# Kernel optimization log

Hardware: AMD Instinct MI355X
Metric: run time of the kernel (lower is better)

## Reference

```python
import jax, jax.numpy as jnp
import numpy as np

# MSEObserver config: bit=4, symmetric=False, ch_axis=-1
QMIN, QMAX = 0, 15          # asymmetric int4: [0, 2^4 - 1]
NUM = 100                   # range-grid resolution
EPS = np.float32(np.finfo(np.float32).eps)


def setup_inputs() -> dict:
    key = jax.random.key(0)
    x_orig = jax.random.normal(key, (1024, 4096), dtype=jnp.float32)
    return {"x_orig": x_orig}


def _search_2d(x):
    # per-tensor (ch_axis == -1) 2D grid search over (range, zero_point)
    x_min = jnp.min(x)
    x_max = jnp.max(x)
    xrange = x_max - x_min
    qrange = float(QMAX - QMIN)
    zps = jnp.arange(QMIN, QMAX + 1, dtype=jnp.float32)  # [Z] candidate zp shifts

    def step(carry, i):
        best_score, best_min, best_max = carry
        tmp_max = xrange / NUM * i           # tmp_min == 0
        tmp_delta = tmp_max / qrange
        new_min = jnp.maximum(-zps * tmp_delta, x_min)           # [Z]
        new_max = jnp.minimum(tmp_max - zps * tmp_delta, x_max)  # [Z]
        # calculate_qparams (asymmetric)
        min_neg = jnp.minimum(new_min, 0.0)
        max_pos = jnp.maximum(new_max, 0.0)
        scale = jnp.maximum((max_pos - min_neg) / qrange, EPS)   # [Z]
        zp = jnp.clip(QMIN - jnp.round(min_neg / scale), QMIN, QMAX)  # [Z]
        s = scale[:, None, None]
        z = zp[:, None, None]
        # fake_quantize_per_tensor_affine, vectorized over Z candidates
        xq = (jnp.clip(jnp.round(x[None] / s) + z, QMIN, QMAX) - z) * s  # [Z,T,D]
        score = jnp.mean(jnp.square(xq - x[None]), axis=(1, 2))  # [Z], lp_loss p=2
        j = jnp.argmin(score)
        sc = score[j]
        better = sc < best_score
        best_min = jnp.where(better, new_min[j], best_min)
        best_max = jnp.where(better, new_max[j], best_max)
        best_score = jnp.minimum(best_score, sc)
        return (best_score, best_min, best_max), None

    init = (jnp.float32(1e10), x_min, x_max)
    iis = jnp.arange(1, NUM + 1, dtype=jnp.float32)
    (best_score, best_min, best_max), _ = jax.lax.scan(step, init, iis)
    return best_min, best_max


def reference(x_orig) -> jnp.ndarray:
    # randn input => one_side_dist == 'no', symmetric == False -> perform_2D_search
    x = x_orig.astype(jnp.float32)
    best_min, best_max = _search_2d(x)
    # buffer update: min_val = min(+inf, best_min), max_val = max(-inf, best_max)
    return jnp.stack([best_min, best_max])
```

## Files before the change

kernel.cpp:

```cpp
#include <hip/hip_runtime.h>
#include <math.h>

#define NUM_I 100
#define NZ    16
#define NCAND (NUM_I * NZ)
#define NBL   8192
#define G2    256
#define BLK   1024
#define SLICE 16384
#define BPT   (NBL / BLK)
#define F32_EPS 1.1920928955078125e-07f
#define AGENT __HIP_MEMORY_SCOPE_AGENT

struct WSL {
    unsigned* ctrs;
    double*   score;
    float*    pmin; float* pmax;
    float4*   params; float2* ranges; float* mm;
    double*   scoreFB;
    size_t    small_needed;
};

__host__ __device__ static inline WSL make_ws(char* w0) {
    WSL L; char* w = w0;
    L.ctrs   = (unsigned*)w; w += 64;
    L.score  = (double*)w;   w += sizeof(double) * NCAND;
    L.pmin   = (float*)w;    w += sizeof(float) * G2;
    L.pmax   = (float*)w;    w += sizeof(float) * G2;
    L.params = (float4*)w;   w += sizeof(float4) * NCAND;
    L.ranges = (float2*)w;   w += sizeof(float2) * NCAND;
    L.mm     = (float*)w;    w += sizeof(float) * 4;
    size_t head = (size_t)(w - w0);
    L.small_needed = (head + 15) & ~(size_t)15;
    L.scoreFB = L.score;
    return L;
}

static __device__ __forceinline__ float rfl_f(float v) {
    return __int_as_float(__builtin_amdgcn_readfirstlane(__float_as_int(v)));
}
static __device__ __forceinline__ double agent_load_f64(const double* p) {
    return __hip_atomic_load(p, __ATOMIC_RELAXED, AGENT);
}
static __device__ __forceinline__ int bin_loc(float v, float lo, float invw) {
    int b = (int)floorf((v - lo) * invw);
    return min(max(b, 0), NBL - 1);
}
static __device__ __forceinline__ void gbar(unsigned* ctr, int nblk) {
    __syncthreads();
    if (threadIdx.x == 0) {
        __hip_atomic_fetch_add(ctr, 1u, __ATOMIC_ACQ_REL, AGENT);
        while (__hip_atomic_load(ctr, __ATOMIC_RELAXED, AGENT) < (unsigned)nblk)
            __builtin_amdgcn_s_sleep(8);
        (void)__hip_atomic_load(ctr, __ATOMIC_ACQUIRE, AGENT);
    }
    __syncthreads();
}

__global__ __launch_bounds__(BLK, 4) void k_fused(const float* __restrict__ x, int n4,
                                                  char* wsbase, float* __restrict__ out) {
    WSL L = make_ws(wsbase);
    __shared__ __align__(16) float ssort[SLICE];
    __shared__ __align__(8) unsigned short Cs[NBL + 2];
    __shared__ __align__(16) double S1p[NBL];
    __shared__ double   dpart[BLK];
    __shared__ unsigned upart[BLK];
    __shared__ double   stot[1];
    __shared__ float    sxm[2];
    __shared__ int      islast;
    unsigned* Htmp = (unsigned*)S1p;
    const int tid = threadIdx.x, blk = blockIdx.x;
    const float4* x4 = (const float4*)x;
    const int per4 = (n4 + G2 - 1) / G2;
    const int beg4 = blk * per4, end4 = min(beg4 + per4, n4);
    const int len = (end4 > beg4) ? (end4 - beg4) * 4 : 0;

    {
        int gtid = blk * BLK + tid;
        if (gtid < NCAND) L.score[gtid] = 0.0;
        float* rmin = (float*)dpart; float* rmax = rmin + BLK;
        float lmin = 3.0e38f, lmax = -3.0e38f;
        for (int i = beg4 + tid; i < end4; i += BLK) {
            float4 v = x4[i];
            lmin = fminf(lmin, fminf(fminf(v.x, v.y), fminf(v.z, v.w)));
            lmax = fmaxf(lmax, fmaxf(fmaxf(v.x, v.y), fmaxf(v.z, v.w)));
        }
        rmin[tid] = lmin; rmax[tid] = lmax;
        __syncthreads();
        for (int s = BLK / 2; s > 0; s >>= 1) {
            if (tid < s) {
                rmin[tid] = fminf(rmin[tid], rmin[tid + s]);
                rmax[tid] = fmaxf(rmax[tid], rmax[tid + s]);
            }
            __syncthreads();
        }
        if (tid == 0) { L.pmin[blk] = rmin[0]; L.pmax[blk] = rmax[0]; }
    }
    gbar(&L.ctrs[0], G2);

    {
        float* rmin = (float*)dpart; float* rmax = rmin + BLK;
        float lmin = (tid < G2) ? L.pmin[tid] : 3.0e38f;
        float lmax = (tid < G2) ? L.pmax[tid] : -3.0e38f;
        rmin[tid] = lmin; rmax[tid] = lmax;
        __syncthreads();
        for (int s = BLK / 2; s > 0; s >>= 1) {
            if (tid < s) {
                rmin[tid] = fminf(rmin[tid], rmin[tid + s]);
                rmax[tid] = fmaxf(rmax[tid], rmax[tid + s]);
            }
            __syncthreads();
        }
        if (tid == 0) { sxm[0] = rmin[0]; sxm[1] = rmax[0]; }
        __syncthreads();
    }
    const float x_min = sxm[0], x_max = sxm[1];
    const float rangef = x_max - x_min;
    const float lo = x_min;
    const float invw = (rangef > 0.0f) ? ((float)NBL / rangef) : 0.0f;

    if (len > 0) {
        for (int b = tid; b < NBL; b += BLK) Htmp[b] = 0u;
        __syncthreads();
        for (int i = beg4 + tid; i < end4; i += BLK) {
            float4 v = x4[i];
            atomicAdd(&Htmp[bin_loc(v.x, lo, invw)], 1u);
            atomicAdd(&Htmp[bin_loc(v.y, lo, invw)], 1u);
            atomicAdd(&Htmp[bin_loc(v.z, lo, invw)], 1u);
            atomicAdd(&Htmp[bin_loc(v.w, lo, invw)], 1u);
        }
        __syncthreads();
        unsigned cl[BPT]; unsigned ps = 0;
        #pragma unroll
        for (int k = 0; k < BPT; k++) { cl[k] = Htmp[tid * BPT + k]; ps += cl[k]; }
        upart[tid] = ps;
        __syncthreads();
        for (int off = 1; off < BLK; off <<= 1) {
            unsigned v = (tid >= off) ? upart[tid - off] : 0u;
            __syncthreads();
            upart[tid] += v;
            __syncthreads();
        }
        unsigned run = upart[tid] - ps;
        #pragma unroll
        for (int k = 0; k < BPT; k++) {
            int b = tid * BPT + k;
            Cs[b] = (unsigned short)run;
            Htmp[b] = run;
            run += cl[k];
        }
        if (tid == BLK - 1) Cs[NBL] = (unsigned short)run;
        __syncthreads();
        for (int i = beg4 + tid; i < end4; i += BLK) {
            float4 v = x4[i];
            unsigned p;
            p = atomicAdd(&Htmp[bin_loc(v.x, lo, invw)], 1u); ssort[p] = v.x;
            p = atomicAdd(&Htmp[bin_loc(v.y, lo, invw)], 1u); ssort[p] = v.y;
            p = atomicAdd(&Htmp[bin_loc(v.z, lo, invw)], 1u); ssort[p] = v.z;
            p = atomicAdd(&Htmp[bin_loc(v.w, lo, invw)], 1u); ssort[p] = v.w;
        }
        __syncthreads();
        for (int k = 0; k < BPT; k++) {
            int b = tid + k * BLK;
            unsigned st = Cs[b], en = Cs[b + 1];
            double s1 = 0.0;
            for (unsigned i = st; i < en; i++) s1 += (double)ssort[i];
            S1p[b] = s1;
        }
        __syncthreads();
        double l1[BPT];
        double a1 = 0.0;
        #pragma unroll
        for (int k = 0; k < BPT; k++) { l1[k] = S1p[tid * BPT + k]; a1 += l1[k]; }
        dpart[tid] = a1;
        __syncthreads();
        for (int off = 1; off < BLK; off <<= 1) {
            double v1 = (tid >= off) ? dpart[tid - off] : 0.0;
            __syncthreads();
            dpart[tid] += v1;
            __syncthreads();
        }
        double b1 = dpart[tid] - a1;
        #pragma unroll
        for (int k = 0; k < BPT; k++) {
            int b = tid * BPT + k;
            S1p[b] = b1; b1 += l1[k];
        }
        if (tid == BLK - 1) stot[0] = dpart[BLK - 1];
        __syncthreads();

        const double totS1 = stot[0];
        for (int q = 0; q < (NCAND + BLK - 1) / BLK; q++) {
            int cand = q * BLK + ((tid + blk) & (BLK - 1));
            if (cand >= NCAND) continue;
            int zi; double sd;
            {
#pragma clang fp contract(off)
                float step = rangef / 100.0f;
                int ii = cand >> 4, z = cand & 15;
                float fi = (float)(ii + 1);
                float tmp_max   = step * fi;
                float tmp_delta = tmp_max / 15.0f;
                float t = (float)z * tmp_delta;
                float new_min = fmaxf(-t, x_min);
                float new_max = fminf(tmp_max - t, x_max);
                float min_neg = fminf(new_min, 0.0f);
                float max_pos = fmaxf(new_max, 0.0f);
                float scale = fmaxf((max_pos - min_neg) / 15.0f, F32_EPS);
                float zp = 0.0f - rintf(min_neg / scale);
                zp = fminf(fmaxf(zp, 0.0f), 15.0f);
                zi = (int)zp; sd = (double)scale;
            }
            double prevC = 0.0, prev1 = 0.0, sc = 0.0;
            for (int j = 0; j <= 15; j++) {
                double Cc, C1;
                if (j < 15) {
                    double td = ((double)(j - zi) + 0.5) * sd;
                    float tf = (float)td;
                    int bf = bin_loc(tf, lo, invw);
                    unsigned st = Cs[bf], en = Cs[bf + 1];
                    unsigned cnt = 0; double s1 = 0.0;
                    unsigned i = st;
                    for (; i < en && (i & 3u); i++) {
                        float v = ssort[i];
                        if (v < tf) { cnt++; s1 += (double)v; }
                    }
                    for (; i + 4u <= en; i += 4u) {
                        float4 v4 = *reinterpret_cast<const float4*>(&ssort[i]);
                        float m0 = (v4.x < tf) ? v4.x : 0.0f;
                        float m1 = (v4.y < tf) ? v4.y : 0.0f;
                        float m2 = (v4.z < tf) ? v4.z : 0.0f;
                        float m3 = (v4.w < tf) ? v4.w : 0.0f;
                        cnt += (v4.x < tf); cnt += (v4.y < tf);
                        cnt += (v4.z < tf); cnt += (v4.w < tf);
                        s1 += (double)((m0 + m1) + (m2 + m3));
                    }
                    for (; i < en; i++) {
                        float v = ssort[i];
                        if (v < tf) { cnt++; s1 += (double)v; }
                    }
                    Cc = (double)st + (double)cnt;
                    C1 = S1p[bf] + s1;
                } else {
                    Cc = (double)len; C1 = totS1;
                }
                double ms = (double)(j - zi) * sd;
                sc += ms * (ms * (Cc - prevC) - 2.0 * (C1 - prev1));
                prevC = Cc; prev1 = C1;
            }
            atomicAdd(&L.score[cand], sc);
        }
    }

    __syncthreads();
    if (tid == 0) {
        __threadfence();
        unsigned old = atomicAdd(&L.ctrs[1], 1u);
        islast = (old == gridDim.x - 1) ? 1 : 0;
    }
    __syncthreads();
    if (!islast) return;
    __threadfence();

    double* bsc = dpart;
    int*    bix = (int*)upart;
    double best = 1.0e300; int bidx = 0x7fffffff;
    for (int c = tid; c < NCAND; c += BLK) {
        double sc = agent_load_f64(&L.score[c]);
        if (sc < best) { best = sc; bidx = c; }
    }
    bsc[tid] = best; bix[tid] = bidx;
    __syncthreads();
    for (int s = BLK / 2; s > 0; s >>= 1) {
        if (tid < s) {
            double so = bsc[tid + s]; int io = bix[tid + s];
            if (so < bsc[tid] || (so == bsc[tid] && io < bix[tid])) { bsc[tid] = so; bix[tid] = io; }
        }
        __syncthreads();
    }
    if (tid == 0) {
        float bmin = x_min, bmax = x_max;
        if (bix[0] != 0x7fffffff) {
#pragma clang fp contract(off)
            int cand = bix[0];
            float step = rangef / 100.0f;
            int ii = cand >> 4, z = cand & 15;
            float fi = (float)(ii + 1);
            float tmp_max   = step * fi;
            float tmp_delta = tmp_max / 15.0f;
            float t = (float)z * tmp_delta;
            bmin = fmaxf(-t, x_min);
            bmax = fminf(tmp_max - t, x_max);
        }
        out[0] = bmin; out[1] = bmax;
    }
}

__global__ __launch_bounds__(256) void k_params_fb(const float* __restrict__ x, int n4,
                                                   float4* __restrict__ params,
                                                   float2* __restrict__ ranges,
                                                   double* __restrict__ score,
                                                   float* __restrict__ mm) {
#pragma clang fp contract(off)
    __shared__ float smin[256], smax[256];
    const float4* x4 = (const float4*)x;
    float lmin = 3.0e38f, lmax = -3.0e38f;
    for (int i = threadIdx.x; i < n4; i += 256) {
        float4 v = x4[i];
        lmin = fminf(lmin, fminf(fminf(v.x, v.y), fminf(v.z, v.w)));
        lmax = fmaxf(lmax, fmaxf(fmaxf(v.x, v.y), fmaxf(v.z, v.w)));
    }
    smin[threadIdx.x] = lmin; smax[threadIdx.x] = lmax;
    __syncthreads();
    for (int s = 128; s > 0; s >>= 1) {
        if (threadIdx.x < s) {
            smin[threadIdx.x] = fminf(smin[threadIdx.x], smin[threadIdx.x + s]);
            smax[threadIdx.x] = fmaxf(smax[threadIdx.x], smax[threadIdx.x + s]);
        }
        __syncthreads();
    }
    float x_min = smin[0], x_max = smax[0];
    if (threadIdx.x == 0) { mm[0] = x_min; mm[1] = x_max; }
    float xrange = x_max - x_min;
    float step = xrange / 100.0f;
    for (int c = threadIdx.x; c < NCAND; c += 256) {
        int ii = c >> 4;
        int z  = c & 15;
        float fi = (float)(ii + 1);
        float tmp_max   = step * fi;
        float tmp_delta = tmp_max / 15.0f;
        float t = (float)z * tmp_delta;
        float new_min = fmaxf(-t, x_min);
        float new_max = fminf(tmp_max - t, x_max);
        float min_neg = fminf(new_min, 0.0f);
        float max_pos = fmaxf(new_max, 0.0f);
        float scale = fmaxf((max_pos - min_neg) / 15.0f, F32_EPS);
        float zp = 0.0f - rintf(min_neg / scale);
        zp = fminf(fmaxf(zp, 0.0f), 15.0f);
        float inv = (float)(1.0 / (double)scale);
        params[c] = make_float4(scale, inv, 0.0f - zp, 15.0f - zp);
        ranges[c] = make_float2(new_min, new_max);
        score[c]  = 0.0;
    }
}

__global__ __launch_bounds__(256) void k_score_bf(const float* __restrict__ x, int n4,
                                                  const float4* __restrict__ params,
                                                  double* __restrict__ score) {
    const int tid = blockIdx.x * 256 + threadIdx.x;
    const int T = gridDim.x * 256;
    const float4* x4 = (const float4*)x;
    float xs[16];
    #pragma unroll
    for (int k = 0; k < 4; k++) {
        int i4 = tid + k * T;
        float4 v;
        if (i4 < n4) v = x4[i4];
        else { v.x = 0.0f; v.y = 0.0f; v.z = 0.0f; v.w = 0.0f; }
        xs[4*k+0] = v.x; xs[4*k+1] = v.y; xs[4*k+2] = v.z; xs[4*k+3] = v.w;
    }
    int c = (int)((blockIdx.x * 37u) % NCAND);
    for (int k = 0; k < NCAND; k++) {
        float4 p = params[c];
        float s   = rfl_f(p.x);
        float inv = rfl_f(p.y);
        float lo  = rfl_f(p.z);
        float hi  = rfl_f(p.w);
        float acc = 0.0f;
        #pragma unroll
        for (int e = 0; e < 16; e++) {
            float r = rintf(xs[e] * inv);
            r = fminf(fmaxf(r, lo), hi);
            float d = fmaf(r, s, -xs[e]);
            acc = fmaf(d, d, acc);
        }
        #pragma unroll
        for (int off = 32; off > 0; off >>= 1)
            acc += __shfl_xor(acc, off);
        if ((threadIdx.x & 63) == 0)
            atomicAdd(&score[c], (double)acc);
        c++; if (c >= NCAND) c -= NCAND;
    }
}

__global__ void k_final_fb(const double* __restrict__ score,
                           const float2* __restrict__ ranges,
                           const float* __restrict__ mm,
                           float* __restrict__ out) {
    if (blockIdx.x == 0 && threadIdx.x == 0) {
        double best = 1.0e300;
        float bmin = mm[0], bmax = mm[1];
        for (int c = 0; c < NCAND; c++) {
            double sc = score[c];
            if (sc < best) { best = sc; bmin = ranges[c].x; bmax = ranges[c].y; }
        }
        out[0] = bmin;
        out[1] = bmax;
    }
}

extern "C" void kernel_launch(void* const* d_in, const int* in_sizes, int n_in,
                              void* d_out, int out_size, void* d_ws, size_t ws_size,
                              hipStream_t stream) {
    const float* x = (const float*)d_in[0];
    int n  = in_sizes[0];
    int n4 = n / 4;
    float* out = (float*)d_out;
    WSL L = make_ws((char*)d_ws);

    int per4 = (n4 + G2 - 1) / G2;
    bool ok = (ws_size >= L.small_needed) && ((n % 4) == 0) && (per4 * 4 <= SLICE) && (n4 > 0);

    if (ok) {
        hipMemsetAsync(d_ws, 0, 64, stream);
        k_fused<<<G2, BLK, 0, stream>>>(x, n4, (char*)d_ws, out);
    } else if (ws_size >= L.small_needed) {
        k_params_fb<<<1, 256, 0, stream>>>(x, n4, L.params, L.ranges, L.scoreFB, L.mm);
        int blocks = ((n4 + 3) / 4 + 255) / 256;
        k_score_bf<<<blocks, 256, 0, stream>>>(x, n4, L.params, L.scoreFB);
        k_final_fb<<<1, 64, 0, stream>>>(L.scoreFB, L.ranges, L.mm, out);
    }
}
```

Before: 129.7 us.

## Use wave shuffles for block reductions/scans and cache input slice in registers

```diff
diff --git a/kernel.cpp b/kernel.cpp
--- a/kernel.cpp
+++ b/kernel.cpp
@@ -8,6 +8,8 @@
 #define G2    256
 #define BLK   1024
 #define SLICE 16384
+#define EPT   16
+#define LPT   4
 #define BPT   (NBL / BLK)
 #define F32_EPS 1.1920928955078125e-07f
 #define AGENT __HIP_MEMORY_SCOPE_AGENT
@@ -63,55 +65,66 @@
     __shared__ __align__(16) float ssort[SLICE];
     __shared__ __align__(8) unsigned short Cs[NBL + 2];
     __shared__ __align__(16) double S1p[NBL];
-    __shared__ double   dpart[BLK];
-    __shared__ unsigned upart[BLK];
+    __shared__ unsigned wsu[16];
+    __shared__ double   wsd[16];
+    __shared__ float    wminf[16], wmaxf[16];
     __shared__ double   stot[1];
     __shared__ float    sxm[2];
     __shared__ int      islast;
     unsigned* Htmp = (unsigned*)S1p;
     const int tid = threadIdx.x, blk = blockIdx.x;
+    const int lane = tid & 63, wv = tid >> 6;
     const float4* x4 = (const float4*)x;
     const int per4 = (n4 + G2 - 1) / G2;
     const int beg4 = blk * per4, end4 = min(beg4 + per4, n4);
     const int len = (end4 > beg4) ? (end4 - beg4) * 4 : 0;
 
+    float xs[EPT];
     {
         int gtid = blk * BLK + tid;
         if (gtid < NCAND) L.score[gtid] = 0.0;
-        float* rmin = (float*)dpart; float* rmax = rmin + BLK;
         float lmin = 3.0e38f, lmax = -3.0e38f;
-        for (int i = beg4 + tid; i < end4; i += BLK) {
-            float4 v = x4[i];
-            lmin = fminf(lmin, fminf(fminf(v.x, v.y), fminf(v.z, v.w)));
-            lmax = fmaxf(lmax, fmaxf(fmaxf(v.x, v.y), fmaxf(v.z, v.w)));
-        }
-        rmin[tid] = lmin; rmax[tid] = lmax;
-        __syncthreads();
-        for (int s = BLK / 2; s > 0; s >>= 1) {
-            if (tid < s) {
-                rmin[tid] = fminf(rmin[tid], rmin[tid + s]);
-                rmax[tid] = fmaxf(rmax[tid], rmax[tid + s]);
-            }
-            __syncthreads();
-        }
-        if (tid == 0) { L.pmin[blk] = rmin[0]; L.pmax[blk] = rmax[0]; }
+        #pragma unroll
+        for (int k = 0; k < LPT; k++) {
+            int i = beg4 + tid + k * BLK;
+            float4 v;
+            if (i < end4) {
+                v = x4[i];
+                lmin = fminf(lmin, fminf(fminf(v.x, v.y), fminf(v.z, v.w)));
+                lmax = fmaxf(lmax, fmaxf(fmaxf(v.x, v.y), fmaxf(v.z, v.w)));
+            } else { v.x = 0.0f; v.y = 0.0f; v.z = 0.0f; v.w = 0.0f; }
+            xs[4*k+0] = v.x; xs[4*k+1] = v.y; xs[4*k+2] = v.z; xs[4*k+3] = v.w;
+        }
+        #pragma unroll
+        for (int off = 32; off > 0; off >>= 1) {
+            lmin = fminf(lmin, __shfl_xor(lmin, off));
+            lmax = fmaxf(lmax, __shfl_xor(lmax, off));
+        }
+        if (lane == 0) { wminf[wv] = lmin; wmaxf[wv] = lmax; }
+        __syncthreads();
+        if (tid == 0) {
+            float a = wminf[0], b = wmaxf[0];
+            for (int k = 1; k < 16; k++) { a = fminf(a, wminf[k]); b = fmaxf(b, wmaxf[k]); }
+            L.pmin[blk] = a; L.pmax[blk] = b;
+        }
     }
     gbar(&L.ctrs[0], G2);
 
     {
-        float* rmin = (float*)dpart; float* rmax = rmin + BLK;
         float lmin = (tid < G2) ? L.pmin[tid] : 3.0e38f;
         float lmax = (tid < G2) ? L.pmax[tid] : -3.0e38f;
-        rmin[tid] = lmin; rmax[tid] = lmax;
-        __syncthreads();
-        for (int s = BLK / 2; s > 0; s >>= 1) {
-            if (tid < s) {
-                rmin[tid] = fminf(rmin[tid], rmin[tid + s]);
-                rmax[tid] = fmaxf(rmax[tid], rmax[tid + s]);
-            }
-            __syncthreads();
-        }
-        if (tid == 0) { sxm[0] = rmin[0]; sxm[1] = rmax[0]; }
+        #pragma unroll
+        for (int off = 32; off > 0; off >>= 1) {
+            lmin = fminf(lmin, __shfl_xor(lmin, off));
+            lmax = fmaxf(lmax, __shfl_xor(lmax, off));
+        }
+        if (lane == 0) { wminf[wv] = lmin; wmaxf[wv] = lmax; }
+        __syncthreads();
+        if (tid == 0) {
+            float a = wminf[0], b = wmaxf[0];
+            for (int k = 1; k < 16; k++) { a = fminf(a, wminf[k]); b = fmaxf(b, wmaxf[k]); }
+            sxm[0] = a; sxm[1] = b;
+        }
         __syncthreads();
     }
     const float x_min = sxm[0], x_max = sxm[1];
@@ -120,44 +133,64 @@
     const float invw = (rangef > 0.0f) ? ((float)NBL / rangef) : 0.0f;
 
     if (len > 0) {
+        unsigned short bins[EPT];
+        #pragma unroll
+        for (int e = 0; e < EPT; e++) bins[e] = (unsigned short)bin_loc(xs[e], lo, invw);
+
         for (int b = tid; b < NBL; b += BLK) Htmp[b] = 0u;
         __syncthreads();
-        for (int i = beg4 + tid; i < end4; i += BLK) {
-            float4 v = x4[i];
-            atomicAdd(&Htmp[bin_loc(v.x, lo, invw)], 1u);
-            atomicAdd(&Htmp[bin_loc(v.y, lo, invw)], 1u);
-            atomicAdd(&Htmp[bin_loc(v.z, lo, invw)], 1u);
-            atomicAdd(&Htmp[bin_loc(v.w, lo, invw)], 1u);
-        }
-        __syncthreads();
-        unsigned cl[BPT]; unsigned ps = 0;
-        #pragma unroll
-        for (int k = 0; k < BPT; k++) { cl[k] = Htmp[tid * BPT + k]; ps += cl[k]; }
-        upart[tid] = ps;
-        __syncthreads();
-        for (int off = 1; off < BLK; off <<= 1) {
-            unsigned v = (tid >= off) ? upart[tid - off] : 0u;
-            __syncthreads();
-            upart[tid] += v;
-            __syncthreads();
-        }
-        unsigned run = upart[tid] - ps;
-        #pragma unroll
-        for (int k = 0; k < BPT; k++) {
-            int b = tid * BPT + k;
-            Cs[b] = (unsigned short)run;
-            Htmp[b] = run;
-            run += cl[k];
-        }
-        if (tid == BLK - 1) Cs[NBL] = (unsigned short)run;
-        __syncthreads();
-        for (int i = beg4 + tid; i < end4; i += BLK) {
-            float4 v = x4[i];
-            unsigned p;
-            p = atomicAdd(&Htmp[bin_loc(v.x, lo, invw)], 1u); ssort[p] = v.x;
-            p = atomicAdd(&Htmp[bin_loc(v.y, lo, invw)], 1u); ssort[p] = v.y;
-            p = atomicAdd(&Htmp[bin_loc(v.z, lo, invw)], 1u); ssort[p] = v.z;
-            p = atomicAdd(&Htmp[bin_loc(v.w, lo, invw)], 1u); ssort[p] = v.w;
+        #pragma unroll
+        for (int k = 0; k < LPT; k++) {
+            if (beg4 + tid + k * BLK < end4) {
+                atomicAdd(&Htmp[bins[4*k+0]], 1u);
+                atomicAdd(&Htmp[bins[4*k+1]], 1u);
+                atomicAdd(&Htmp[bins[4*k+2]], 1u);
+                atomicAdd(&Htmp[bins[4*k+3]], 1u);
+            }
+        }
+        __syncthreads();
+        {
+            unsigned cl[BPT]; unsigned ps = 0;
+            #pragma unroll
+            for (int k = 0; k < BPT; k++) { cl[k] = Htmp[tid * BPT + k]; ps += cl[k]; }
+            unsigned incl = ps;
+            #pragma unroll
+            for (int off = 1; off < 64; off <<= 1) {
+                unsigned t = __shfl_up(incl, off);
+                if (lane >= off) incl += t;
+            }
+            if (lane == 63) wsu[wv] = incl;
+            __syncthreads();
+            if (wv == 0 && lane < 16) {
+                unsigned w = wsu[lane], wi = w;
+                #pragma unroll
+                for (int off = 1; off < 16; off <<= 1) {
+                    unsigned t = __shfl_up(wi, off);
+                    if (lane >= off) wi += t;
+                }
+                wsu[lane] = wi - w;
+            }
+            __syncthreads();
+            unsigned run = wsu[wv] + incl - ps;
+            #pragma unroll
+            for (int k = 0; k < BPT; k++) {
+                int b = tid * BPT + k;
+                Cs[b] = (unsigned short)run;
+                Htmp[b] = run;
+                run += cl[k];
+            }
+            if (tid == BLK - 1) Cs[NBL] = (unsigned short)run;
+            __syncthreads();
+        }
+        #pragma unroll
+        for (int k = 0; k < LPT; k++) {
+            if (beg4 + tid + k * BLK < end4) {
+                unsigned p;
+                p = atomicAdd(&Htmp[bins[4*k+0]], 1u); ssort[p] = xs[4*k+0];
+                p = atomicAdd(&Htmp[bins[4*k+1]], 1u); ssort[p] = xs[4*k+1];
+                p = atomicAdd(&Htmp[bins[4*k+2]], 1u); ssort[p] = xs[4*k+2];
+                p = atomicAdd(&Htmp[bins[4*k+3]], 1u); ssort[p] = xs[4*k+3];
+            }
         }
         __syncthreads();
         for (int k = 0; k < BPT; k++) {
@@ -168,26 +201,37 @@
             S1p[b] = s1;
         }
         __syncthreads();
-        double l1[BPT];
-        double a1 = 0.0;
-        #pragma unroll
-        for (int k = 0; k < BPT; k++) { l1[k] = S1p[tid * BPT + k]; a1 += l1[k]; }
-        dpart[tid] = a1;
-        __syncthreads();
-        for (int off = 1; off < BLK; off <<= 1) {
-            double v1 = (tid >= off) ? dpart[tid - off] : 0.0;
-            __syncthreads();
-            dpart[tid] += v1;
-            __syncthreads();
-        }
-        double b1 = dpart[tid] - a1;
-        #pragma unroll
-        for (int k = 0; k < BPT; k++) {
-            int b = tid * BPT + k;
-            S1p[b] = b1; b1 += l1[k];
-        }
-        if (tid == BLK - 1) stot[0] = dpart[BLK - 1];
-        __syncthreads();
+        {
+            double l1[BPT]; double a1 = 0.0;
+            #pragma unroll
+            for (int k = 0; k < BPT; k++) { l1[k] = S1p[tid * BPT + k]; a1 += l1[k]; }
+            double incl = a1;
+            #pragma unroll
+            for (int off = 1; off < 64; off <<= 1) {
+                double t = __shfl_up(incl, off);
+                if (lane >= off) incl += t;
+            }
+            if (lane == 63) wsd[wv] = incl;
+            __syncthreads();
+            if (wv == 0 && lane < 16) {
+                double w = wsd[lane], wi = w;
+                #pragma unroll
+                for (int off = 1; off < 16; off <<= 1) {
+                    double t = __shfl_up(wi, off);
+                    if (lane >= off) wi += t;
+                }
+                wsd[lane] = wi - w;
+            }
+            __syncthreads();
+            double b1 = wsd[wv] + incl - a1;
+            #pragma unroll
+            for (int k = 0; k < BPT; k++) {
+                int b = tid * BPT + k;
+                S1p[b] = b1; b1 += l1[k];
+            }
+            if (tid == BLK - 1) stot[0] = b1;
+            __syncthreads();
+        }
 
         const double totS1 = stot[0];
         for (int q = 0; q < (NCAND + BLK - 1) / BLK; q++) {
@@ -262,29 +306,29 @@
     if (!islast) return;
     __threadfence();
 
-    double* bsc = dpart;
-    int*    bix = (int*)upart;
     double best = 1.0e300; int bidx = 0x7fffffff;
     for (int c = tid; c < NCAND; c += BLK) {
         double sc = agent_load_f64(&L.score[c]);
         if (sc < best) { best = sc; bidx = c; }
     }
-    bsc[tid] = best; bix[tid] = bidx;
-    __syncthreads();
-    for (int s = BLK / 2; s > 0; s >>= 1) {
-        if (tid < s) {
-            double so = bsc[tid + s]; int io = bix[tid + s];
-            if (so < bsc[tid] || (so == bsc[tid] && io < bix[tid])) { bsc[tid] = so; bix[tid] = io; }
-        }
-        __syncthreads();
-    }
+    #pragma unroll
+    for (int off = 32; off > 0; off >>= 1) {
+        double so = __shfl_xor(best, off); int io = __shfl_xor(bidx, off);
+        if (so < best || (so == best && io < bidx)) { best = so; bidx = io; }
+    }
+    if (lane == 0) { wsd[wv] = best; wsu[wv] = (unsigned)bidx; }
+    __syncthreads();
     if (tid == 0) {
+        double bs = wsd[0]; int bi = (int)wsu[0];
+        for (int k = 1; k < 16; k++) {
+            double so = wsd[k]; int io = (int)wsu[k];
+            if (so < bs || (so == bs && io < bi)) { bs = so; bi = io; }
+        }
         float bmin = x_min, bmax = x_max;
-        if (bix[0] != 0x7fffffff) {
+        if (bi != 0x7fffffff) {
 #pragma clang fp contract(off)
-            int cand = bix[0];
             float step = rangef / 100.0f;
-            int ii = cand >> 4, z = cand & 15;
+            int ii = bi >> 4, z = bi & 15;
             float fi = (float)(ii + 1);
             float tmp_max   = step * fi;
             float tmp_delta = tmp_max / 15.0f;
```

Result: faster. 125.9 us (-2.9%).
